# Performance work log

Measured on AMD Instinct MI355X. Metric: run time of the kernel, lower is better.

The kernel has to match this reference:

```python
import jax, jax.numpy as jnp
import numpy as np

N, E = 100000, 400000
IN, HID, H, D = 165, 128, 8, 16  # per-head dim D = HID // H
NUM_CLASSES = 2


def layer_norm(x, g, b, eps=1e-5):
    m = jnp.mean(x, axis=-1, keepdims=True)
    v = jnp.var(x, axis=-1, keepdims=True)
    return (x - m) / jnp.sqrt(v + eps) * g + b


def transformer_conv(x, src, dst, Wq, bq, Wk, bk, Wv, bv, Ws, bs):
    # x: [N, HID]; src/dst: [E]
    n = x.shape[0]
    q = (x @ Wq + bq).reshape(n, H, D)
    k = (x @ Wk + bk).reshape(n, H, D)
    v = (x @ Wv + bv).reshape(n, H, D)
    # per-edge attention logits: [E, H]
    alpha = jnp.sum(q[dst] * k[src], axis=-1) / jnp.sqrt(jnp.float32(D))
    # segment softmax over incoming edges of each destination node
    amax = jax.ops.segment_max(alpha, dst, num_segments=n)          # [N, H]
    amax = jnp.where(jnp.isfinite(amax), amax, 0.0)
    ex = jnp.exp(alpha - amax[dst])                                  # [E, H]
    denom = jax.ops.segment_sum(ex, dst, num_segments=n)            # [N, H]
    a = ex / (denom[dst] + 1e-16)
    msg = v[src] * a[..., None]                                      # [E, H, D]
    out = jax.ops.segment_sum(msg, dst, num_segments=n)             # [N, H, D]
    out = out.reshape(n, H * D)
    # root skip connection (root_weight=True, beta=False in PyG defaults)
    return out + x @ Ws + bs


def setup_inputs() -> dict:
    key = jax.random.key(0)
    ks = jax.random.split(key, 24)
    rn = lambda k, s: (jax.random.normal(k, s, jnp.float32) * 0.05)
    inp = {
        "x": jax.random.normal(ks[0], (N, IN), jnp.float32),
        "edge_index": jax.random.randint(ks[1], (2, E), 0, N, jnp.int32),
        "W_in": rn(ks[2], (IN, HID)), "b_in": jnp.zeros((HID,), jnp.float32),
        # layer 1 TransformerConv
        "Wq1": rn(ks[3], (HID, HID)), "bq1": jnp.zeros((HID,), jnp.float32),
        "Wk1": rn(ks[4], (HID, HID)), "bk1": jnp.zeros((HID,), jnp.float32),
        "Wv1": rn(ks[5], (HID, HID)), "bv1": jnp.zeros((HID,), jnp.float32),
        "Ws1": rn(ks[6], (HID, HID)), "bs1": jnp.zeros((HID,), jnp.float32),
        "g1": jnp.ones((HID,), jnp.float32), "be1": jnp.zeros((HID,), jnp.float32),
        # layer 2 TransformerConv
        "Wq2": rn(ks[7], (HID, HID)), "bq2": jnp.zeros((HID,), jnp.float32),
        "Wk2": rn(ks[8], (HID, HID)), "bk2": jnp.zeros((HID,), jnp.float32),
        "Wv2": rn(ks[9], (HID, HID)), "bv2": jnp.zeros((HID,), jnp.float32),
        "Ws2": rn(ks[10], (HID, HID)), "bs2": jnp.zeros((HID,), jnp.float32),
        "g2": jnp.ones((HID,), jnp.float32), "be2": jnp.zeros((HID,), jnp.float32),
        # classifier MLP
        "Wc1": rn(ks[11], (HID, HID // 2)), "bc1": jnp.zeros((HID // 2,), jnp.float32),
        "Wc2": rn(ks[12], (HID // 2, NUM_CLASSES)), "bc2": jnp.zeros((NUM_CLASSES,), jnp.float32),
    }
    return inp


def reference(x, edge_index, W_in, b_in,
              Wq1, bq1, Wk1, bk1, Wv1, bv1, Ws1, bs1, g1, be1,
              Wq2, bq2, Wk2, bk2, Wv2, bv2, Ws2, bs2, g2, be2,
              Wc1, bc1, Wc2, bc2):
    src, dst = edge_index[0], edge_index[1]
    h = x @ W_in + b_in                                   # input projection
    h_new = transformer_conv(h, src, dst, Wq1, bq1, Wk1, bk1, Wv1, bv1, Ws1, bs1)
    h = layer_norm(h + h_new, g1, be1)                    # dropout = identity (eval)
    h_new = transformer_conv(h, src, dst, Wq2, bq2, Wk2, bk2, Wv2, bv2, Ws2, bs2)
    h = layer_norm(h + h_new, g2, be2)
    return jax.nn.relu(h @ Wc1 + bc1) @ Wc2 + bc2         # [N, num_classes]
```

## Files before the change

kernel.cpp:

```cpp
#include <hip/hip_runtime.h>
#include <hip/hip_bf16.h>

#define NN 100000
#define EE 400000
#define IN_DIM 165
#define KPAD 192
#define HID 128
#define C1 64
#define NC 2
#define SCANB 256
#define NBLK 391
#define NBD2 782

typedef const float* fpp;
typedef __hip_bfloat16 bf16;
typedef __attribute__((ext_vector_type(8))) short s16x8;
typedef __attribute__((ext_vector_type(4))) float f32x4;

__device__ __forceinline__ float bflo(unsigned u) { return __uint_as_float(u << 16); }
__device__ __forceinline__ float bfhi(unsigned u) { return __uint_as_float(u & 0xFFFF0000u); }
__device__ __forceinline__ unsigned short bfbits(float f) {
    bf16 h = __float2bfloat16(f);
    return *reinterpret_cast<unsigned short*>(&h);
}

__global__ void k_cvt_weights(fpp W_in, fpp Wq1, fpp Wk1, fpp Wv1, fpp Ws1,
                              fpp Wq2, fpp Wk2, fpp Wv2, fpp Ws2, fpp Wc1,
                              unsigned short* __restrict__ winpack,
                              unsigned short* __restrict__ wpack,
                              unsigned short* __restrict__ wc1t) {
    int idx = blockIdx.x * blockDim.x + threadIdx.x;
    if (idx < 24576) {
        int n = idx / KPAD, k = idx % KPAD;
        float v = (k < IN_DIM) ? W_in[k * HID + n] : 0.f;
        winpack[idx] = bfbits(v);
    } else if (idx < 155648) {
        int local = idx - 24576;
        int j = local >> 14;
        int l14 = local & 16383;
        int n = l14 >> 7, k = l14 & 127;
        const float* src;
        switch (j) {
            case 0: src = Wq1; break; case 1: src = Wk1; break;
            case 2: src = Wv1; break; case 3: src = Ws1; break;
            case 4: src = Wq2; break; case 5: src = Wk2; break;
            case 6: src = Wv2; break; default: src = Ws2; break;
        }
        wpack[local] = bfbits(src[k * HID + n]);
    } else {
        int local = idx - 155648;
        int n = local >> 7, k = local & 127;
        wc1t[local] = bfbits(Wc1[k * C1 + n]);
    }
}

__global__ void k_cvt_x(fpp x, unsigned short* __restrict__ xb) {
    int i = blockIdx.x * blockDim.x + threadIdx.x;
    int row = i / 24, c = i % 24;
    s16x8 us;
#pragma unroll
    for (int j = 0; j < 8; j++) {
        int col = c * 8 + j;
        float v = (col < IN_DIM) ? x[(size_t)row * IN_DIM + col] : 0.f;
        us[j] = (short)bfbits(v);
    }
    *(s16x8*)(xb + (size_t)row * KPAD + c * 8) = us;
}

__global__ void k_deg_zero(int* __restrict__ deg) {
    int i = blockIdx.x * blockDim.x + threadIdx.x;
    if (i < NN) deg[i] = 0;
}
__global__ void k_hist(const int* __restrict__ dst, int* __restrict__ deg) {
    int e = blockIdx.x * blockDim.x + threadIdx.x;
    if (e < EE) atomicAdd(&deg[dst[e]], 1);
}
__global__ void k_scan1(const int* __restrict__ deg, int* __restrict__ pos,
                        int* __restrict__ bsum, int n) {
    __shared__ int tmp[SCANB];
    int t = threadIdx.x, i = blockIdx.x * SCANB + t;
    int v = (i < n) ? deg[i] : 0;
    tmp[t] = v; __syncthreads();
    for (int off = 1; off < SCANB; off <<= 1) {
        int x = (t >= off) ? tmp[t - off] : 0;
        __syncthreads();
        tmp[t] += x;
        __syncthreads();
    }
    if (i < n) pos[i] = tmp[t] - v;
    if (t == SCANB - 1) bsum[blockIdx.x] = tmp[t];
}
__global__ void k_scan2(int* __restrict__ bsum, int nb) {
    __shared__ int tmp[512];
    int t = threadIdx.x;
    int v = (t < nb) ? bsum[t] : 0;
    tmp[t] = v; __syncthreads();
    for (int off = 1; off < 512; off <<= 1) {
        int x = (t >= off) ? tmp[t - off] : 0;
        __syncthreads();
        tmp[t] += x;
        __syncthreads();
    }
    if (t < nb) bsum[t] = tmp[t] - v;
}
__global__ void k_scan3(int* __restrict__ pos, const int* __restrict__ bsum, int n) {
    int i = blockIdx.x * blockDim.x + threadIdx.x;
    if (i < n) pos[i] += bsum[blockIdx.x];
}
__global__ void k_fill(const int* __restrict__ src, const int* __restrict__ dst,
                       int* __restrict__ pos, int* __restrict__ esrc) {
    int e = blockIdx.x * blockDim.x + threadIdx.x;
    if (e < EE) {
        int p = atomicAdd(&pos[dst[e]], 1);
        esrc[p] = src[e];
    }
}

__global__ __launch_bounds__(256) void k_dense_in(const unsigned short* __restrict__ xb,
                                                  const unsigned short* __restrict__ winpack,
                                                  fpp b_in, float* __restrict__ h) {
    __shared__ unsigned short As[128 * 72];
    __shared__ unsigned short Ws[128 * 72];
    int row0 = blockIdx.x * 128;
    int t = threadIdx.x, lane = t & 63, w = t >> 6;
    int quad = lane >> 4, l16 = lane & 15;
    int m_off = (w >> 1) * 64, n_off = (w & 1) * 64;

    f32x4 acc[4][4];
    float bias_v[4];
#pragma unroll
    for (int ni = 0; ni < 4; ni++) bias_v[ni] = b_in[n_off + ni * 16 + l16];
#pragma unroll
    for (int mi = 0; mi < 4; mi++)
#pragma unroll
        for (int ni = 0; ni < 4; ni++)
            acc[mi][ni] = (f32x4){bias_v[ni], bias_v[ni], bias_v[ni], bias_v[ni]};

    for (int kc = 0; kc < 3; kc++) {
        __syncthreads();
        for (int i = 0; i < 4; i++) {
            int g = t + i * 256;
            int r = g >> 3, c = g & 7;
            int rg = min(row0 + r, NN - 1);
            *(s16x8*)(As + r * 72 + c * 8) =
                *(const s16x8*)(xb + (size_t)rg * KPAD + kc * 64 + c * 8);
            *(s16x8*)(Ws + r * 72 + c * 8) =
                *(const s16x8*)(winpack + r * KPAD + kc * 64 + c * 8);
        }
        __syncthreads();
#pragma unroll
        for (int ks = 0; ks < 2; ks++) {
            int k0 = ks * 32;
            s16x8 a[4], b[4];
#pragma unroll
            for (int mi = 0; mi < 4; mi++)
                a[mi] = *(const s16x8*)(As + (m_off + mi * 16 + l16) * 72 + k0 + quad * 8);
#pragma unroll
            for (int ni = 0; ni < 4; ni++)
                b[ni] = *(const s16x8*)(Ws + (n_off + ni * 16 + l16) * 72 + k0 + quad * 8);
#pragma unroll
            for (int mi = 0; mi < 4; mi++)
#pragma unroll
                for (int ni = 0; ni < 4; ni++)
                    acc[mi][ni] = __builtin_amdgcn_mfma_f32_16x16x32_bf16(
                        a[mi], b[ni], acc[mi][ni], 0, 0, 0);
        }
    }
#pragma unroll
    for (int mi = 0; mi < 4; mi++)
#pragma unroll
        for (int ni = 0; ni < 4; ni++)
#pragma unroll
            for (int r = 0; r < 4; r++) {
                int m = row0 + m_off + mi * 16 + quad * 4 + r;
                if (m < NN)
                    h[(size_t)m * HID + n_off + ni * 16 + l16] = acc[mi][ni][r];
            }
}

__global__ __launch_bounds__(256) void k_dense4(const float* __restrict__ h,
                                                const unsigned short* __restrict__ wpackL,
                                                fpp bq, fpp bk, fpp bv, fpp bs,
                                                bf16* __restrict__ qb, bf16* __restrict__ kb,
                                                bf16* __restrict__ vb, bf16* __restrict__ agg) {
    __shared__ unsigned short As[128 * 136];
    __shared__ unsigned short Ws[128 * 136];
    int row0 = blockIdx.x * 128;
    int t = threadIdx.x, lane = t & 63, w = t >> 6;
    int quad = lane >> 4, l16 = lane & 15;
    int m_off = (w >> 1) * 64, n_off = (w & 1) * 64;

    for (int i = 0; i < 8; i++) {
        int g = t + i * 256;
        int r = g >> 4, c = g & 15;
        int rg = min(row0 + r, NN - 1);
        float4 f0 = *(const float4*)(h + (size_t)rg * HID + c * 8);
        float4 f1 = *(const float4*)(h + (size_t)rg * HID + c * 8 + 4);
        s16x8 us;
        us[0] = (short)bfbits(f0.x); us[1] = (short)bfbits(f0.y);
        us[2] = (short)bfbits(f0.z); us[3] = (short)bfbits(f0.w);
        us[4] = (short)bfbits(f1.x); us[5] = (short)bfbits(f1.y);
        us[6] = (short)bfbits(f1.z); us[7] = (short)bfbits(f1.w);
        *(s16x8*)(As + r * 136 + c * 8) = us;
    }
    __syncthreads();

    s16x8 afr[4][4];
#pragma unroll
    for (int ks = 0; ks < 4; ks++)
#pragma unroll
        for (int mi = 0; mi < 4; mi++)
            afr[ks][mi] = *(const s16x8*)(As + (m_off + mi * 16 + l16) * 136 + ks * 32 + quad * 8);

    for (int nc = 0; nc < 4; nc++) {
        const float* bp; bf16* tp;
        if (nc == 0)      { bp = bq; tp = qb; }
        else if (nc == 1) { bp = bk; tp = kb; }
        else if (nc == 2) { bp = bv; tp = vb; }
        else              { bp = bs; tp = agg; }

        __syncthreads();
        for (int i = 0; i < 8; i++) {
            int g = t + i * 256;
            int r = g >> 4, c = g & 15;
            *(s16x8*)(Ws + r * 136 + c * 8) =
                *(const s16x8*)(wpackL + nc * 16384 + r * HID + c * 8);
        }
        __syncthreads();

        f32x4 acc[4][4];
        float bias_v[4];
#pragma unroll
        for (int ni = 0; ni < 4; ni++) bias_v[ni] = bp[n_off + ni * 16 + l16];
#pragma unroll
        for (int mi = 0; mi < 4; mi++)
#pragma unroll
            for (int ni = 0; ni < 4; ni++)
                acc[mi][ni] = (f32x4){bias_v[ni], bias_v[ni], bias_v[ni], bias_v[ni]};

#pragma unroll
        for (int ks = 0; ks < 4; ks++) {
            s16x8 b[4];
#pragma unroll
            for (int ni = 0; ni < 4; ni++)
                b[ni] = *(const s16x8*)(Ws + (n_off + ni * 16 + l16) * 136 + ks * 32 + quad * 8);
#pragma unroll
            for (int mi = 0; mi < 4; mi++)
#pragma unroll
                for (int ni = 0; ni < 4; ni++)
                    acc[mi][ni] = __builtin_amdgcn_mfma_f32_16x16x32_bf16(
                        afr[ks][mi], b[ni], acc[mi][ni], 0, 0, 0);
        }
        __syncthreads();

        unsigned short* Cs = Ws;
#pragma unroll
        for (int mi = 0; mi < 4; mi++)
#pragma unroll
            for (int ni = 0; ni < 4; ni++)
#pragma unroll
                for (int r = 0; r < 4; r++)
                    Cs[(m_off + mi * 16 + quad * 4 + r) * 136 + n_off + ni * 16 + l16] =
                        bfbits(acc[mi][ni][r]);
        __syncthreads();
        for (int i = 0; i < 8; i++) {
            int g = t + i * 256;
            int r = g >> 4, c = g & 15;
            if (row0 + r < NN)
                *(s16x8*)((unsigned short*)tp + (size_t)(row0 + r) * HID + c * 8) =
                    *(const s16x8*)(Cs + r * 136 + c * 8);
        }
    }
}

__global__ void k_agg_ln(const bf16* __restrict__ qb, const bf16* __restrict__ kb,
                         const bf16* __restrict__ vb, const int* __restrict__ pos,
                         const int* __restrict__ deg, const int* __restrict__ esrc,
                         const bf16* __restrict__ agg, float* __restrict__ h,
                         fpp g, fpp b) {
    int wid = (blockIdx.x * blockDim.x + threadIdx.x) >> 6;
    if (wid >= NN) return;
    int lane = threadIdx.x & 63;
    int d = wid;
    unsigned qu = ((const unsigned*)(qb + (size_t)d * HID))[lane];
    float q0 = bflo(qu) * 0.25f, q1 = bfhi(qu) * 0.25f;
    int cnt = deg[d];
    int start = pos[d] - cnt;
    float m = -INFINITY, L = 0.f, o0 = 0.f, o1 = 0.f;
    for (int base = 0; base < cnt; base += 64) {
        int nc = min(64, cnt - base);
        int sj = (lane < nc) ? esrc[start + base + lane] : 0;
        int j = 0;
        for (; j + 1 < nc; j += 2) {
            int s0 = __shfl(sj, j, 64);
            int s1 = __shfl(sj, j + 1, 64);
            unsigned ku0 = ((const unsigned*)(kb + (size_t)s0 * HID))[lane];
            unsigned ku1 = ((const unsigned*)(kb + (size_t)s1 * HID))[lane];
            unsigned vu0 = ((const unsigned*)(vb + (size_t)s0 * HID))[lane];
            unsigned vu1 = ((const unsigned*)(vb + (size_t)s1 * HID))[lane];
            float t0 = q0 * bflo(ku0) + q1 * bfhi(ku0);
            float t1 = q0 * bflo(ku1) + q1 * bfhi(ku1);
            t0 += __shfl_xor(t0, 1, 64); t1 += __shfl_xor(t1, 1, 64);
            t0 += __shfl_xor(t0, 2, 64); t1 += __shfl_xor(t1, 2, 64);
            t0 += __shfl_xor(t0, 4, 64); t1 += __shfl_xor(t1, 4, 64);
            float nm = fmaxf(m, fmaxf(t0, t1));
            float corr = __expf(m - nm);
            float p0 = __expf(t0 - nm), p1 = __expf(t1 - nm);
            L = L * corr + p0 + p1;
            o0 = o0 * corr + p0 * bflo(vu0) + p1 * bflo(vu1);
            o1 = o1 * corr + p0 * bfhi(vu0) + p1 * bfhi(vu1);
            m = nm;
        }
        if (j < nc) {
            int s0 = __shfl(sj, j, 64);
            unsigned ku0 = ((const unsigned*)(kb + (size_t)s0 * HID))[lane];
            unsigned vu0 = ((const unsigned*)(vb + (size_t)s0 * HID))[lane];
            float t0 = q0 * bflo(ku0) + q1 * bfhi(ku0);
            t0 += __shfl_xor(t0, 1, 64);
            t0 += __shfl_xor(t0, 2, 64);
            t0 += __shfl_xor(t0, 4, 64);
            float nm = fmaxf(m, t0);
            float corr = __expf(m - nm);
            float p0 = __expf(t0 - nm);
            L = L * corr + p0;
            o0 = o0 * corr + p0 * bflo(vu0);
            o1 = o1 * corr + p0 * bfhi(vu0);
            m = nm;
        }
    }
    float inv = 1.f / (L + 1e-16f);
    unsigned au = ((const unsigned*)(agg + (size_t)d * HID))[lane];
    float2 hv = ((const float2*)(h + (size_t)d * HID))[lane];
    float v0 = hv.x + bflo(au) + o0 * inv;
    float v1 = hv.y + bfhi(au) + o1 * inv;
    float s = v0 + v1, s2 = v0 * v0 + v1 * v1;
    for (int off = 32; off; off >>= 1) {
        s += __shfl_xor(s, off, 64);
        s2 += __shfl_xor(s2, off, 64);
    }
    float mn = s * (1.f / HID);
    float var = s2 * (1.f / HID) - mn * mn;
    float invs = rsqrtf(var + 1e-5f);
    float2 gv = ((const float2*)g)[lane];
    float2 bv = ((const float2*)b)[lane];
    float2 o;
    o.x = (v0 - mn) * invs * gv.x + bv.x;
    o.y = (v1 - mn) * invs * gv.y + bv.y;
    ((float2*)(h + (size_t)d * HID))[lane] = o;
}

__global__ __launch_bounds__(256) void k_classifier(const float* __restrict__ h,
                                                    const unsigned short* __restrict__ wc1t,
                                                    fpp bc1, fpp Wc2, fpp bc2,
                                                    float* __restrict__ out) {
    __shared__ unsigned short As[128 * 136];
    __shared__ unsigned short Ws[64 * 136];
    int row0 = blockIdx.x * 128;
    int t = threadIdx.x, lane = t & 63, w = t >> 6;
    int quad = lane >> 4, l16 = lane & 15;
    int m_off = w * 32;

    for (int i = 0; i < 8; i++) {
        int g = t + i * 256;
        int r = g >> 4, c = g & 15;
        int rg = min(row0 + r, NN - 1);
        float4 f0 = *(const float4*)(h + (size_t)rg * HID + c * 8);
        float4 f1 = *(const float4*)(h + (size_t)rg * HID + c * 8 + 4);
        s16x8 us;
        us[0] = (short)bfbits(f0.x); us[1] = (short)bfbits(f0.y);
        us[2] = (short)bfbits(f0.z); us[3] = (short)bfbits(f0.w);
        us[4] = (short)bfbits(f1.x); us[5] = (short)bfbits(f1.y);
        us[6] = (short)bfbits(f1.z); us[7] = (short)bfbits(f1.w);
        *(s16x8*)(As + r * 136 + c * 8) = us;
    }
    for (int i = 0; i < 4; i++) {
        int g = t + i * 256;
        int r = g >> 4, c = g & 15;
        *(s16x8*)(Ws + r * 136 + c * 8) = *(const s16x8*)(wc1t + r * HID + c * 8);
    }
    __syncthreads();

    f32x4 acc[2][4];
    float bias_v[4];
#pragma unroll
    for (int ni = 0; ni < 4; ni++) bias_v[ni] = bc1[ni * 16 + l16];
#pragma unroll
    for (int mi = 0; mi < 2; mi++)
#pragma unroll
        for (int ni = 0; ni < 4; ni++)
            acc[mi][ni] = (f32x4){bias_v[ni], bias_v[ni], bias_v[ni], bias_v[ni]};

#pragma unroll
    for (int ks = 0; ks < 4; ks++) {
        s16x8 a[2], b[4];
#pragma unroll
        for (int mi = 0; mi < 2; mi++)
            a[mi] = *(const s16x8*)(As + (m_off + mi * 16 + l16) * 136 + ks * 32 + quad * 8);
#pragma unroll
        for (int ni = 0; ni < 4; ni++)
            b[ni] = *(const s16x8*)(Ws + (ni * 16 + l16) * 136 + ks * 32 + quad * 8);
#pragma unroll
        for (int mi = 0; mi < 2; mi++)
#pragma unroll
            for (int ni = 0; ni < 4; ni++)
                acc[mi][ni] = __builtin_amdgcn_mfma_f32_16x16x32_bf16(
                    a[mi], b[ni], acc[mi][ni], 0, 0, 0);
    }
    __syncthreads();
    float* Cs = (float*)As;
#pragma unroll
    for (int mi = 0; mi < 2; mi++)
#pragma unroll
        for (int ni = 0; ni < 4; ni++)
#pragma unroll
            for (int r = 0; r < 4; r++)
                Cs[(m_off + mi * 16 + quad * 4 + r) * 68 + ni * 16 + l16] =
                    fmaxf(acc[mi][ni][r], 0.f);
    __syncthreads();

    int row = t >> 1, half = t & 1;
    float p0 = 0.f, p1 = 0.f;
    for (int c = half * 32; c < half * 32 + 32; c++) {
        float v = Cs[row * 68 + c];
        p0 += v * Wc2[c * NC + 0];
        p1 += v * Wc2[c * NC + 1];
    }
    p0 += __shfl_xor(p0, 1, 64);
    p1 += __shfl_xor(p1, 1, 64);
    if (half == 0 && row0 + row < NN) {
        out[(size_t)(row0 + row) * NC + 0] = p0 + bc2[0];
        out[(size_t)(row0 + row) * NC + 1] = p1 + bc2[1];
    }
}

extern "C" void kernel_launch(void* const* d_in, const int* in_sizes, int n_in,
                              void* d_out, int out_size, void* d_ws, size_t ws_size,
                              hipStream_t stream) {
    fpp x = (fpp)d_in[0];
    const int* ei = (const int*)d_in[1];
    const int* src = ei;
    const int* dst = ei + EE;
    fpp W_in = (fpp)d_in[2];  fpp b_in = (fpp)d_in[3];
    fpp Wq1 = (fpp)d_in[4];   fpp bq1 = (fpp)d_in[5];
    fpp Wk1 = (fpp)d_in[6];   fpp bk1 = (fpp)d_in[7];
    fpp Wv1 = (fpp)d_in[8];   fpp bv1 = (fpp)d_in[9];
    fpp Ws1 = (fpp)d_in[10];  fpp bs1 = (fpp)d_in[11];
    fpp g1 = (fpp)d_in[12];   fpp be1 = (fpp)d_in[13];
    fpp Wq2 = (fpp)d_in[14];  fpp bq2 = (fpp)d_in[15];
    fpp Wk2 = (fpp)d_in[16];  fpp bk2 = (fpp)d_in[17];
    fpp Wv2 = (fpp)d_in[18];  fpp bv2 = (fpp)d_in[19];
    fpp Ws2 = (fpp)d_in[20];  fpp bs2 = (fpp)d_in[21];
    fpp g2 = (fpp)d_in[22];   fpp be2 = (fpp)d_in[23];
    fpp Wc1 = (fpp)d_in[24];  fpp bc1 = (fpp)d_in[25];
    fpp Wc2 = (fpp)d_in[26];  fpp bc2 = (fpp)d_in[27];
    float* out = (float*)d_out;

    char* p = (char*)d_ws;
    float* h = (float*)p;            p += (size_t)NN * HID * 4;
    bf16* agg = (bf16*)p;            p += (size_t)NN * HID * 2;
    bf16* qb = (bf16*)p;             p += (size_t)NN * HID * 2;
    bf16* kb = (bf16*)p;             p += (size_t)NN * HID * 2;
    bf16* vb = (bf16*)p;             p += (size_t)NN * HID * 2;
    int* deg = (int*)p;              p += (size_t)NN * 4;
    int* pos = (int*)p;              p += (size_t)NN * 4;
    int* esrc = (int*)p;             p += (size_t)EE * 4;
    int* bsum = (int*)p;             p += 512 * 4;
    unsigned short* winpack = (unsigned short*)p;  p += 24576 * 2;
    unsigned short* wpack = (unsigned short*)p;    p += 131072 * 2;
    unsigned short* wc1t = (unsigned short*)p;     p += 8192 * 2;
    unsigned short* xb = (unsigned short*)qb;

    const int nE = (EE + 255) / 256;
    const int nNn = (NN + 255) / 256;

    k_cvt_weights<<<640, 256, 0, stream>>>(W_in, Wq1, Wk1, Wv1, Ws1,
                                           Wq2, Wk2, Wv2, Ws2, Wc1,
                                           winpack, wpack, wc1t);
    k_cvt_x<<<9375, 256, 0, stream>>>(x, xb);

    k_deg_zero<<<nNn, 256, 0, stream>>>(deg);
    k_hist<<<nE, 256, 0, stream>>>(dst, deg);
    k_scan1<<<NBLK, SCANB, 0, stream>>>(deg, pos, bsum, NN);
    k_scan2<<<1, 512, 0, stream>>>(bsum, NBLK);
    k_scan3<<<NBLK, SCANB, 0, stream>>>(pos, bsum, NN);
    k_fill<<<nE, 256, 0, stream>>>(src, dst, pos, esrc);

    k_dense_in<<<NBD2, 256, 0, stream>>>(xb, winpack, b_in, h);

    for (int layer = 0; layer < 2; layer++) {
        fpp bq = layer ? bq2 : bq1, bk = layer ? bk2 : bk1;
        fpp bv = layer ? bv2 : bv1, bs = layer ? bs2 : bs1;
        fpp g = layer ? g2 : g1, be = layer ? be2 : be1;
        const unsigned short* wpackL = wpack + (size_t)layer * 65536;

        k_dense4<<<NBD2, 256, 0, stream>>>(h, wpackL, bq, bk, bv, bs, qb, kb, vb, agg);
        k_agg_ln<<<(NN * 64 + 255) / 256, 256, 0, stream>>>(qb, kb, vb, pos, deg, esrc,
                                                            agg, h, g, be);
    }

    k_classifier<<<NBD2, 256, 0, stream>>>(h, wc1t, bc1, Wc2, bc2, out);
}
```

Measured before the change: 448.9 us.

## Store hidden state in bf16 and pack CSR start/count into int2

The fp32 hidden-state buffer h becomes a bf16 buffer. The input projection writes it through an LDS-staged coalesced store, and the dense, aggregation/layernorm and classifier kernels read and write bf16 directly, without per-element conversion from fp32. This halves hidden-state traffic, at the cost of rounding the residual path and layernorm output to bf16. It also packs each node's CSR start and count into one int2 so the aggregation kernel does a single load per node, and it replaces the zeroing kernel with hipMemsetAsync.

```diff
diff --git a/kernel.cpp b/kernel.cpp
--- a/kernel.cpp
+++ b/kernel.cpp
@@ -67,10 +67,6 @@
     *(s16x8*)(xb + (size_t)row * KPAD + c * 8) = us;
 }
 
-__global__ void k_deg_zero(int* __restrict__ deg) {
-    int i = blockIdx.x * blockDim.x + threadIdx.x;
-    if (i < NN) deg[i] = 0;
-}
 __global__ void k_hist(const int* __restrict__ dst, int* __restrict__ deg) {
     int e = blockIdx.x * blockDim.x + threadIdx.x;
     if (e < EE) atomicAdd(&deg[dst[e]], 1);
@@ -115,12 +111,21 @@
         esrc[p] = src[e];
     }
 }
+__global__ void k_pack_csr(const int* __restrict__ pos, const int* __restrict__ deg,
+                           int2* __restrict__ csr2) {
+    int i = blockIdx.x * blockDim.x + threadIdx.x;
+    if (i < NN) {
+        int c = deg[i];
+        csr2[i] = make_int2(pos[i] - c, c);
+    }
+}
 
 __global__ __launch_bounds__(256) void k_dense_in(const unsigned short* __restrict__ xb,
                                                   const unsigned short* __restrict__ winpack,
-                                                  fpp b_in, float* __restrict__ h) {
-    __shared__ unsigned short As[128 * 72];
-    __shared__ unsigned short Ws[128 * 72];
+                                                  fpp b_in, unsigned short* __restrict__ hb) {
+    __shared__ unsigned short smem[18432];
+    unsigned short* As = smem;
+    unsigned short* Ws = smem + 9216;
     int row0 = blockIdx.x * 128;
     int t = threadIdx.x, lane = t & 63, w = t >> 6;
     int quad = lane >> 4, l16 = lane & 15;
@@ -166,19 +171,27 @@
                         a[mi], b[ni], acc[mi][ni], 0, 0, 0);
         }
     }
+    __syncthreads();
+    unsigned short* Cs = smem;
 #pragma unroll
     for (int mi = 0; mi < 4; mi++)
 #pragma unroll
         for (int ni = 0; ni < 4; ni++)
 #pragma unroll
-            for (int r = 0; r < 4; r++) {
-                int m = row0 + m_off + mi * 16 + quad * 4 + r;
-                if (m < NN)
-                    h[(size_t)m * HID + n_off + ni * 16 + l16] = acc[mi][ni][r];
-            }
-}
-
-__global__ __launch_bounds__(256) void k_dense4(const float* __restrict__ h,
+            for (int r = 0; r < 4; r++)
+                Cs[(m_off + mi * 16 + quad * 4 + r) * 136 + n_off + ni * 16 + l16] =
+                    bfbits(acc[mi][ni][r]);
+    __syncthreads();
+    for (int i = 0; i < 8; i++) {
+        int g = t + i * 256;
+        int r = g >> 4, c = g & 15;
+        if (row0 + r < NN)
+            *(s16x8*)(hb + (size_t)(row0 + r) * HID + c * 8) =
+                *(const s16x8*)(Cs + r * 136 + c * 8);
+    }
+}
+
+__global__ __launch_bounds__(256) void k_dense4(const unsigned short* __restrict__ hb,
                                                 const unsigned short* __restrict__ wpackL,
                                                 fpp bq, fpp bk, fpp bv, fpp bs,
                                                 bf16* __restrict__ qb, bf16* __restrict__ kb,
@@ -194,14 +207,7 @@
         int g = t + i * 256;
         int r = g >> 4, c = g & 15;
         int rg = min(row0 + r, NN - 1);
-        float4 f0 = *(const float4*)(h + (size_t)rg * HID + c * 8);
-        float4 f1 = *(const float4*)(h + (size_t)rg * HID + c * 8 + 4);
-        s16x8 us;
-        us[0] = (short)bfbits(f0.x); us[1] = (short)bfbits(f0.y);
-        us[2] = (short)bfbits(f0.z); us[3] = (short)bfbits(f0.w);
-        us[4] = (short)bfbits(f1.x); us[5] = (short)bfbits(f1.y);
-        us[6] = (short)bfbits(f1.z); us[7] = (short)bfbits(f1.w);
-        *(s16x8*)(As + r * 136 + c * 8) = us;
+        *(s16x8*)(As + r * 136 + c * 8) = *(const s16x8*)(hb + (size_t)rg * HID + c * 8);
     }
     __syncthreads();
 
@@ -274,18 +280,17 @@
 }
 
 __global__ void k_agg_ln(const bf16* __restrict__ qb, const bf16* __restrict__ kb,
-                         const bf16* __restrict__ vb, const int* __restrict__ pos,
-                         const int* __restrict__ deg, const int* __restrict__ esrc,
-                         const bf16* __restrict__ agg, float* __restrict__ h,
-                         fpp g, fpp b) {
+                         const bf16* __restrict__ vb, const int2* __restrict__ csr2,
+                         const int* __restrict__ esrc, const bf16* __restrict__ agg,
+                         unsigned short* __restrict__ hb, fpp g, fpp b) {
     int wid = (blockIdx.x * blockDim.x + threadIdx.x) >> 6;
     if (wid >= NN) return;
     int lane = threadIdx.x & 63;
     int d = wid;
     unsigned qu = ((const unsigned*)(qb + (size_t)d * HID))[lane];
     float q0 = bflo(qu) * 0.25f, q1 = bfhi(qu) * 0.25f;
-    int cnt = deg[d];
-    int start = pos[d] - cnt;
+    int2 se = csr2[d];
+    int start = se.x, cnt = se.y;
     float m = -INFINITY, L = 0.f, o0 = 0.f, o1 = 0.f;
     for (int base = 0; base < cnt; base += 64) {
         int nc = min(64, cnt - base);
@@ -330,9 +335,9 @@
     }
     float inv = 1.f / (L + 1e-16f);
     unsigned au = ((const unsigned*)(agg + (size_t)d * HID))[lane];
-    float2 hv = ((const float2*)(h + (size_t)d * HID))[lane];
-    float v0 = hv.x + bflo(au) + o0 * inv;
-    float v1 = hv.y + bfhi(au) + o1 * inv;
+    unsigned hu = ((const unsigned*)(hb + (size_t)d * HID))[lane];
+    float v0 = bflo(hu) + bflo(au) + o0 * inv;
+    float v1 = bfhi(hu) + bfhi(au) + o1 * inv;
     float s = v0 + v1, s2 = v0 * v0 + v1 * v1;
     for (int off = 32; off; off >>= 1) {
         s += __shfl_xor(s, off, 64);
@@ -343,13 +348,12 @@
     float invs = rsqrtf(var + 1e-5f);
     float2 gv = ((const float2*)g)[lane];
     float2 bv = ((const float2*)b)[lane];
-    float2 o;
-    o.x = (v0 - mn) * invs * gv.x + bv.x;
-    o.y = (v1 - mn) * invs * gv.y + bv.y;
-    ((float2*)(h + (size_t)d * HID))[lane] = o;
-}
-
-__global__ __launch_bounds__(256) void k_classifier(const float* __restrict__ h,
+    float ox = (v0 - mn) * invs * gv.x + bv.x;
+    float oy = (v1 - mn) * invs * gv.y + bv.y;
+    ((unsigned*)(hb + (size_t)d * HID))[lane] = ((unsigned)bfbits(oy) << 16) | bfbits(ox);
+}
+
+__global__ __launch_bounds__(256) void k_classifier(const unsigned short* __restrict__ hb,
                                                     const unsigned short* __restrict__ wc1t,
                                                     fpp bc1, fpp Wc2, fpp bc2,
                                                     float* __restrict__ out) {
@@ -364,14 +368,7 @@
         int g = t + i * 256;
         int r = g >> 4, c = g & 15;
         int rg = min(row0 + r, NN - 1);
-        float4 f0 = *(const float4*)(h + (size_t)rg * HID + c * 8);
-        float4 f1 = *(const float4*)(h + (size_t)rg * HID + c * 8 + 4);
-        s16x8 us;
-        us[0] = (short)bfbits(f0.x); us[1] = (short)bfbits(f0.y);
-        us[2] = (short)bfbits(f0.z); us[3] = (short)bfbits(f0.w);
-        us[4] = (short)bfbits(f1.x); us[5] = (short)bfbits(f1.y);
-        us[6] = (short)bfbits(f1.z); us[7] = (short)bfbits(f1.w);
-        *(s16x8*)(As + r * 136 + c * 8) = us;
+        *(s16x8*)(As + r * 136 + c * 8) = *(const s16x8*)(hb + (size_t)rg * HID + c * 8);
     }
     for (int i = 0; i < 4; i++) {
         int g = t + i * 256;
@@ -456,13 +453,14 @@
     float* out = (float*)d_out;
 
     char* p = (char*)d_ws;
-    float* h = (float*)p;            p += (size_t)NN * HID * 4;
+    unsigned short* hb = (unsigned short*)p;  p += (size_t)NN * HID * 2;
     bf16* agg = (bf16*)p;            p += (size_t)NN * HID * 2;
     bf16* qb = (bf16*)p;             p += (size_t)NN * HID * 2;
     bf16* kb = (bf16*)p;             p += (size_t)NN * HID * 2;
     bf16* vb = (bf16*)p;             p += (size_t)NN * HID * 2;
     int* deg = (int*)p;              p += (size_t)NN * 4;
     int* pos = (int*)p;              p += (size_t)NN * 4;
+    int2* csr2 = (int2*)p;           p += (size_t)NN * 8;
     int* esrc = (int*)p;             p += (size_t)EE * 4;
     int* bsum = (int*)p;             p += 512 * 4;
     unsigned short* winpack = (unsigned short*)p;  p += 24576 * 2;
@@ -478,14 +476,15 @@
                                            winpack, wpack, wc1t);
     k_cvt_x<<<9375, 256, 0, stream>>>(x, xb);
 
-    k_deg_zero<<<nNn, 256, 0, stream>>>(deg);
+    hipMemsetAsync(deg, 0, (size_t)NN * 4, stream);
     k_hist<<<nE, 256, 0, stream>>>(dst, deg);
     k_scan1<<<NBLK, SCANB, 0, stream>>>(deg, pos, bsum, NN);
     k_scan2<<<1, 512, 0, stream>>>(bsum, NBLK);
     k_scan3<<<NBLK, SCANB, 0, stream>>>(pos, bsum, NN);
     k_fill<<<nE, 256, 0, stream>>>(src, dst, pos, esrc);
-
-    k_dense_in<<<NBD2, 256, 0, stream>>>(xb, winpack, b_in, h);
+    k_pack_csr<<<nNn, 256, 0, stream>>>(pos, deg, csr2);
+
+    k_dense_in<<<NBD2, 256, 0, stream>>>(xb, winpack, b_in, hb);
 
     for (int layer = 0; layer < 2; layer++) {
         fpp bq = layer ? bq2 : bq1, bk = layer ? bk2 : bk1;
@@ -493,10 +492,10 @@
         fpp g = layer ? g2 : g1, be = layer ? be2 : be1;
         const unsigned short* wpackL = wpack + (size_t)layer * 65536;
 
-        k_dense4<<<NBD2, 256, 0, stream>>>(h, wpackL, bq, bk, bv, bs, qb, kb, vb, agg);
-        k_agg_ln<<<(NN * 64 + 255) / 256, 256, 0, stream>>>(qb, kb, vb, pos, deg, esrc,
-                                                            agg, h, g, be);
-    }
-
-    k_classifier<<<NBD2, 256, 0, stream>>>(h, wc1t, bc1, Wc2, bc2, out);
-}
+        k_dense4<<<NBD2, 256, 0, stream>>>(hb, wpackL, bq, bk, bv, bs, qb, kb, vb, agg);
+        k_agg_ln<<<(NN * 64 + 255) / 256, 256, 0, stream>>>(qb, kb, vb, csr2, esrc,
+                                                            agg, hb, g, be);
+    }
+
+    k_classifier<<<NBD2, 256, 0, stream>>>(hb, wc1t, bc1, Wc2, bc2, out);
+}
```

New measurement: 426.5 us. 1.05x faster.
